# Performance work log

Measured on AMD Instinct MI355X. Metric: run time of the kernel, lower is better.

Reference implementation:

```python
import jax, jax.numpy as jnp
import numpy as np

B = 16384          # batch
N_IN = 1024        # input nodes
L = 8              # layers
W_LAYER = 512      # nodes per layer (fan-in and fan-out)
N_NODES = N_IN + L * W_LAYER  # 5120 total nodes in shared buffer
MASK_DENSITY = 0.25


def setup_inputs() -> dict:
    key = jax.random.key(0)
    kx, kw, km, kb = jax.random.split(key, 4)
    x = jax.random.normal(kx, (B, N_IN), dtype=jnp.float32)
    W = jax.random.normal(kw, (L, W_LAYER, W_LAYER), dtype=jnp.float32) * 0.05
    mask = (jax.random.uniform(km, (L, W_LAYER, W_LAYER)) < MASK_DENSITY).astype(jnp.float32)
    bias = jax.random.normal(kb, (L, W_LAYER), dtype=jnp.float32) * 0.01
    rng = np.random.default_rng(0)
    # layer l gathers from nodes already computed: indices in [0, N_IN + l*W_LAYER)
    in_idx = np.stack([rng.integers(0, N_IN + l * W_LAYER, size=W_LAYER) for l in range(L)]).astype(np.int32)
    # layer l writes its own contiguous node slots
    out_idx = np.stack([np.arange(N_IN + l * W_LAYER, N_IN + (l + 1) * W_LAYER) for l in range(L)]).astype(np.int32)
    return {"x": x, "W": W, "mask": mask, "bias": bias,
            "in_idx": jnp.asarray(in_idx), "out_idx": jnp.asarray(out_idx)}


def reference(x, W, mask, bias, in_idx, out_idx):
    # shared node-value buffer, inputs written into first N_IN columns
    values = jnp.zeros((x.shape[0], N_NODES), dtype=x.dtype)
    values = values.at[:, :N_IN].set(x)

    def step(vals, layer):
        idx_in, idx_out, Wl, ml, bl = layer
        node_inputs = vals[:, idx_in]                       # [B, W_LAYER] gather
        h = jax.nn.relu(node_inputs @ (Wl * ml).T + bl)     # masked linear + ReLU
        return vals.at[:, idx_out].set(h), None             # scatter back

    values, _ = jax.lax.scan(step, values, (in_idx, out_idx, W, mask, bias))
    return values[:, out_idx[-1]]  # output nodes = last layer's nodes
```

## Files before the change

### kernel.cpp

```cpp
#include <hip/hip_runtime.h>
#include <stdint.h>

typedef unsigned short u16;
typedef unsigned int   u32;
typedef short s16x8 __attribute__((ext_vector_type(8)));
typedef float f32x4 __attribute__((ext_vector_type(4)));

#define NB    16384
#define NIN   1024
#define WLY   512
#define NLAY  8
#define NNODE (NIN + NLAY * WLY)
#define BN    64

__device__ __forceinline__ u16 f2bf(float f) {
  union { float f; u32 u; } c; c.f = f;
  return (u16)((c.u + 0x7fffu + ((c.u >> 16) & 1u)) >> 16);
}
__device__ __forceinline__ float bf2f(u16 h) {
  union { u32 u; float f; } c; c.u = ((u32)h) << 16;
  return c.f;
}

#define SCHED0() __builtin_amdgcn_sched_barrier(0)
#define BAR()    __builtin_amdgcn_s_barrier()
#define WAITLG0() asm volatile("s_waitcnt lgkmcnt(0)" ::: "memory")

__global__ void prep_w(const float* __restrict__ W, const float* __restrict__ Mk,
                       u16* __restrict__ Wm) {
  int id   = blockIdx.x * 256 + threadIdx.x;
  int lane = id & 63;
  int chunk = id >> 6;
  int kf = chunk & 1;
  int mb = (chunk >> 1) & 31;
  int kt = (chunk >> 6) & 7;
  int l  = chunk >> 9;
  int m  = (mb << 4) + (lane & 15);
  int k0 = (kt << 6) + (kf << 5) + ((lane >> 4) << 3);
  size_t base = ((size_t)l << 18) + (size_t)m * 512 + k0;
  const float4* w4 = (const float4*)(W + base);
  const float4* k4 = (const float4*)(Mk + base);
  float4 w0 = w4[0], w1 = w4[1];
  float4 k0v = k4[0], k1v = k4[1];
  u32 p0 = (u32)f2bf(w0.x * k0v.x) | ((u32)f2bf(w0.y * k0v.y) << 16);
  u32 p1 = (u32)f2bf(w0.z * k0v.z) | ((u32)f2bf(w0.w * k0v.w) << 16);
  u32 p2 = (u32)f2bf(w1.x * k1v.x) | ((u32)f2bf(w1.y * k1v.y) << 16);
  u32 p3 = (u32)f2bf(w1.z * k1v.z) | ((u32)f2bf(w1.w * k1v.w) << 16);
  uint4 v; v.x = p0; v.y = p1; v.z = p2; v.w = p3;
  *(uint4*)(Wm + ((size_t)chunk << 9) + (lane << 3)) = v;
}

__global__ __launch_bounds__(512, 2) void fused_net(
    const float* __restrict__ x, const u16* __restrict__ Wfrag,
    const float* __restrict__ bias, const int* __restrict__ in_idx,
    u16* __restrict__ V, float* __restrict__ out) {

  __shared__ __align__(16) u16 Graw[2][64 * 72];
  __shared__ __align__(16) u16 Gswz[4][4096];
  __shared__ __align__(16) u16 Ebuf[512 * 72];

  int t = threadIdx.x;
  int lane = t & 63, w = t >> 6;
  int mlane = lane & 15, g = lane >> 4;
  int n0 = blockIdx.x * BN;
  int krow  = (w << 3) + (lane >> 3);
  int kcol8 = lane & 7;

  float* xt = (float*)Ebuf;
  for (int cc = 0; cc < 8; ++cc) {
    #pragma unroll
    for (int it = 0; it < 4; ++it) {
      int cl = t + it * 512;
      int b = cl >> 5, p = cl & 31;
      *(float4*)(xt + b * 128 + (p << 2)) =
          *(const float4*)(x + (size_t)(n0 + b) * 1024 + cc * 128 + (p << 2));
    }
    __syncthreads();
    {
      int c = t >> 2, seg = t & 3;
      u32 p[8];
      #pragma unroll
      for (int i = 0; i < 8; ++i) {
        u16 lo = f2bf(xt[(seg * 16 + 2 * i) * 128 + c]);
        u16 hi = f2bf(xt[(seg * 16 + 2 * i + 1) * 128 + c]);
        p[i] = (u32)lo | ((u32)hi << 16);
      }
      u16* dst = V + (size_t)(cc * 128 + c) * NB + n0 + seg * 16;
      uint4 v0; v0.x = p[0]; v0.y = p[1]; v0.z = p[2]; v0.w = p[3];
      uint4 v1; v1.x = p[4]; v1.y = p[5]; v1.z = p[6]; v1.w = p[7];
      *(uint4*)dst = v0;
      *(uint4*)(dst + 8) = v1;
    }
    __syncthreads();
  }

#define GLD(KT) do {                                                           \
    gv[(KT) & 3] =                                                             \
        *(const uint4*)(V + (size_t)rowv[KT] * NB + n0 + (kcol8 << 3));        \
  } while (0)

#define STW(KT) do {                                                           \
    *(uint4*)((char*)Graw[(KT) & 1] + krow * 144 + (kcol8 << 4)) =             \
        gv[(KT) & 3];                                                          \
  } while (0)

#define TRANSP(KT) do {                                                        \
    const u16* gb_ = Graw[(KT) & 1];                                           \
    u32 p0_ = (u32)gb_[(w * 8 + 0) * 72 + lane] |                              \
              ((u32)gb_[(w * 8 + 1) * 72 + lane] << 16);                       \
    u32 p1_ = (u32)gb_[(w * 8 + 2) * 72 + lane] |                              \
              ((u32)gb_[(w * 8 + 3) * 72 + lane] << 16);                       \
    u32 p2_ = (u32)gb_[(w * 8 + 4) * 72 + lane] |                              \
              ((u32)gb_[(w * 8 + 5) * 72 + lane] << 16);                       \
    u32 p3_ = (u32)gb_[(w * 8 + 6) * 72 + lane] |                              \
              ((u32)gb_[(w * 8 + 7) * 72 + lane] << 16);                       \
    uint4 vv_; vv_.x = p0_; vv_.y = p1_; vv_.z = p2_; vv_.w = p3_;             \
    *(uint4*)((char*)Gswz[(KT) & 3] + lane * 128 +                             \
              ((w * 16) ^ ((lane & 7) << 4))) = vv_;                           \
  } while (0)

#define LDA(KTN) do {                                                          \
    _Pragma("unroll") for (int mb = 0; mb < 4; ++mb)                           \
    _Pragma("unroll") for (int kf = 0; kf < 2; ++kf)                           \
      a[(KTN) & 3][mb][kf] = *(const s16x8*)(Wl +                              \
          ((size_t)((((KTN) * 32 + (w << 2) + mb) << 1) + kf) << 9) +          \
          (lane << 3));                                                        \
  } while (0)

#define MM(KT) do {                                                            \
    const char* gs_ = (const char*)Gswz[(KT) & 3];                             \
    _Pragma("unroll") for (int kf = 0; kf < 2; ++kf) {                         \
      s16x8 bfr[4];                                                            \
      _Pragma("unroll") for (int nf = 0; nf < 4; ++nf) {                       \
        int n_ = (nf << 4) + mlane;                                            \
        bfr[nf] = *(const s16x8*)(gs_ + n_ * 128 +                             \
                  (((kf << 6) + (g << 4)) ^ ((n_ & 7) << 4)));                 \
      }                                                                        \
      _Pragma("unroll") for (int mb = 0; mb < 4; ++mb)                         \
      _Pragma("unroll") for (int nf = 0; nf < 4; ++nf)                         \
        acc[mb][nf] = __builtin_amdgcn_mfma_f32_16x16x32_bf16(                 \
            a[(KT) & 3][mb][kf], bfr[nf], acc[mb][nf], 0, 0, 0);               \
    }                                                                          \
  } while (0)

  for (int l = 0; l < NLAY; ++l) {
    __syncthreads();

    int rowv[8];
    #pragma unroll
    for (int kt = 0; kt < 8; ++kt)
      rowv[kt] = in_idx[(l << 9) + (kt << 6) + krow];

    const u16* Wl = Wfrag + ((size_t)l << 18);
    int node_out = NIN + l * WLY;

    f32x4 acc[4][4];
    #pragma unroll
    for (int i = 0; i < 4; ++i)
      #pragma unroll
      for (int j = 0; j < 4; ++j)
        acc[i][j] = (f32x4){0.f, 0.f, 0.f, 0.f};

    s16x8 a[4][4][2];
    uint4 gv[4];

    GLD(0); GLD(1);
    LDA(0); LDA(1);
    STW(0); STW(1);
    TRANSP(0); TRANSP(1);
    GLD(2); GLD(3);
    SCHED0(); WAITLG0(); BAR(); SCHED0();

    GLD(4); GLD(5);
    LDA(2); LDA(3);
    MM(0); MM(1);
    STW(2); STW(3);
    TRANSP(2); TRANSP(3);
    SCHED0(); WAITLG0(); BAR(); SCHED0();

    GLD(6); GLD(7);
    LDA(4); LDA(5);
    MM(2); MM(3);
    STW(4); STW(5);
    TRANSP(4); TRANSP(5);
    SCHED0(); WAITLG0(); BAR(); SCHED0();

    LDA(6); LDA(7);
    MM(4); MM(5);
    STW(6); STW(7);
    TRANSP(6); TRANSP(7);
    SCHED0(); WAITLG0(); BAR(); SCHED0();

    MM(6); MM(7);

    if (l < NLAY - 1) {
      #pragma unroll
      for (int mb = 0; mb < 4; ++mb) {
        float4 bv = *(const float4*)(bias + (l << 9) + (w << 6) + (mb << 4) + (g << 2));
        float bvr[4] = {bv.x, bv.y, bv.z, bv.w};
        #pragma unroll
        for (int nf = 0; nf < 4; ++nf)
          #pragma unroll
          for (int r = 0; r < 4; ++r) {
            int m = (w << 6) + (mb << 4) + (g << 2) + r;
            int n = (nf << 4) + mlane;
            Ebuf[m * 72 + n] = f2bf(fmaxf(acc[mb][nf][r] + bvr[r], 0.f));
          }
      }
      #pragma unroll
      for (int it = 0; it < 8; ++it) {
        int row = (w << 6) + (it << 3) + (lane >> 3);
        uint4 vv = *(uint4*)(Ebuf + row * 72 + ((lane & 7) << 3));
        *(uint4*)(V + (size_t)(node_out + row) * NB + n0 + ((lane & 7) << 3)) = vv;
      }
    } else {
      #pragma unroll
      for (int mb = 0; mb < 4; ++mb) {
        float4 bv = *(const float4*)(bias + (l << 9) + (w << 6) + (mb << 4) + (g << 2));
        float bvr[4] = {bv.x, bv.y, bv.z, bv.w};
        #pragma unroll
        for (int nf = 0; nf < 4; ++nf)
          #pragma unroll
          for (int r = 0; r < 4; ++r) {
            int m = (w << 6) + (mb << 4) + (g << 2) + r;
            int n = (nf << 4) + mlane;
            Ebuf[m * 66 + n] = f2bf(fmaxf(acc[mb][nf][r] + bvr[r], 0.f));
          }
      }
      __syncthreads();
      #pragma unroll
      for (int pn = 0; pn < 8; ++pn)
        #pragma unroll
        for (int h = 0; h < 2; ++h) {
          int n = (t >> 6) + (pn << 3);
          int mbase = ((t & 63) << 2) + (h << 8);
          float4 v;
          v.x = bf2f(Ebuf[(mbase + 0) * 66 + n]);
          v.y = bf2f(Ebuf[(mbase + 1) * 66 + n]);
          v.z = bf2f(Ebuf[(mbase + 2) * 66 + n]);
          v.w = bf2f(Ebuf[(mbase + 3) * 66 + n]);
          *(float4*)(out + (size_t)(n0 + n) * 512 + mbase) = v;
        }
    }
  }
#undef GLD
#undef STW
#undef TRANSP
#undef LDA
#undef MM
}

extern "C" void kernel_launch(void* const* d_in, const int* in_sizes, int n_in,
                              void* d_out, int out_size, void* d_ws, size_t ws_size,
                              hipStream_t stream) {
  (void)in_sizes; (void)n_in; (void)out_size; (void)ws_size;
  const float* x    = (const float*)d_in[0];
  const float* W    = (const float*)d_in[1];
  const float* Mk   = (const float*)d_in[2];
  const float* bias = (const float*)d_in[3];
  const int*  inidx = (const int*)d_in[4];
  float* out = (float*)d_out;

  char* ws = (char*)d_ws;
  u16* V     = (u16*)ws;
  u16* Wfrag = (u16*)(ws + (size_t)NNODE * NB * 2);

  prep_w<<<dim3(1024), 256, 0, stream>>>(W, Mk, Wfrag);
  fused_net<<<dim3(256), 512, 0, stream>>>(x, Wfrag, bias, inidx, V, out);
}
```

Baseline: 108.8 us.

## Double fused_net block to 1024 threads, halve per-wave rows, prefetch next indices

The fused network kernel now runs with 16 waves per block instead of 8. Each wave owns 32 output rows instead of 64 and moves half-width slices of the gathered activations, so accumulator and A-fragment register arrays shrink to keep more waves resident. Weight-fragment loads are now interleaved one k-tile ahead with the MFMA steps rather than staged two at a time. Next-layer gather indices are prefetched during the current layer's matmul. The aim is more latency hiding per CU, at the cost of narrower 8-byte global and LDS accesses and a launch bound that may force tighter register limits or spills.

```diff
diff --git a/kernel.cpp b/kernel.cpp
--- a/kernel.cpp
+++ b/kernel.cpp
@@ -50,7 +50,7 @@
   *(uint4*)(Wm + ((size_t)chunk << 9) + (lane << 3)) = v;
 }
 
-__global__ __launch_bounds__(512, 2) void fused_net(
+__global__ __launch_bounds__(1024, 4) void fused_net(
     const float* __restrict__ x, const u16* __restrict__ Wfrag,
     const float* __restrict__ bias, const int* __restrict__ in_idx,
     u16* __restrict__ V, float* __restrict__ out) {
@@ -63,67 +63,60 @@
   int lane = t & 63, w = t >> 6;
   int mlane = lane & 15, g = lane >> 4;
   int n0 = blockIdx.x * BN;
-  int krow  = (w << 3) + (lane >> 3);
-  int kcol8 = lane & 7;
+  int krow  = (w << 2) + (lane >> 4);
+  int kcol4 = lane & 15;
 
   float* xt = (float*)Ebuf;
   for (int cc = 0; cc < 8; ++cc) {
     #pragma unroll
-    for (int it = 0; it < 4; ++it) {
-      int cl = t + it * 512;
+    for (int it = 0; it < 2; ++it) {
+      int cl = t + it * 1024;
       int b = cl >> 5, p = cl & 31;
       *(float4*)(xt + b * 128 + (p << 2)) =
           *(const float4*)(x + (size_t)(n0 + b) * 1024 + cc * 128 + (p << 2));
     }
     __syncthreads();
     {
-      int c = t >> 2, seg = t & 3;
-      u32 p[8];
-      #pragma unroll
-      for (int i = 0; i < 8; ++i) {
-        u16 lo = f2bf(xt[(seg * 16 + 2 * i) * 128 + c]);
-        u16 hi = f2bf(xt[(seg * 16 + 2 * i + 1) * 128 + c]);
+      int c = t >> 3, seg = t & 7;
+      u32 p[4];
+      #pragma unroll
+      for (int i = 0; i < 4; ++i) {
+        u16 lo = f2bf(xt[(seg * 8 + 2 * i) * 128 + c]);
+        u16 hi = f2bf(xt[(seg * 8 + 2 * i + 1) * 128 + c]);
         p[i] = (u32)lo | ((u32)hi << 16);
       }
-      u16* dst = V + (size_t)(cc * 128 + c) * NB + n0 + seg * 16;
-      uint4 v0; v0.x = p[0]; v0.y = p[1]; v0.z = p[2]; v0.w = p[3];
-      uint4 v1; v1.x = p[4]; v1.y = p[5]; v1.z = p[6]; v1.w = p[7];
-      *(uint4*)dst = v0;
-      *(uint4*)(dst + 8) = v1;
+      uint4 vv; vv.x = p[0]; vv.y = p[1]; vv.z = p[2]; vv.w = p[3];
+      *(uint4*)(V + (size_t)(cc * 128 + c) * NB + n0 + (seg << 3)) = vv;
     }
     __syncthreads();
   }
 
 #define GLD(KT) do {                                                           \
     gv[(KT) & 3] =                                                             \
-        *(const uint4*)(V + (size_t)rowv[KT] * NB + n0 + (kcol8 << 3));        \
+        *(const uint2*)(V + (size_t)rowv[KT] * NB + n0 + (kcol4 << 2));        \
   } while (0)
 
 #define STW(KT) do {                                                           \
-    *(uint4*)((char*)Graw[(KT) & 1] + krow * 144 + (kcol8 << 4)) =             \
+    *(uint2*)((char*)Graw[(KT) & 1] + krow * 144 + (kcol4 << 3)) =             \
         gv[(KT) & 3];                                                          \
   } while (0)
 
 #define TRANSP(KT) do {                                                        \
     const u16* gb_ = Graw[(KT) & 1];                                           \
-    u32 p0_ = (u32)gb_[(w * 8 + 0) * 72 + lane] |                              \
-              ((u32)gb_[(w * 8 + 1) * 72 + lane] << 16);                       \
-    u32 p1_ = (u32)gb_[(w * 8 + 2) * 72 + lane] |                              \
-              ((u32)gb_[(w * 8 + 3) * 72 + lane] << 16);                       \
-    u32 p2_ = (u32)gb_[(w * 8 + 4) * 72 + lane] |                              \
-              ((u32)gb_[(w * 8 + 5) * 72 + lane] << 16);                       \
-    u32 p3_ = (u32)gb_[(w * 8 + 6) * 72 + lane] |                              \
-              ((u32)gb_[(w * 8 + 7) * 72 + lane] << 16);                       \
-    uint4 vv_; vv_.x = p0_; vv_.y = p1_; vv_.z = p2_; vv_.w = p3_;             \
-    *(uint4*)((char*)Gswz[(KT) & 3] + lane * 128 +                             \
-              ((w * 16) ^ ((lane & 7) << 4))) = vv_;                           \
+    u32 p0_ = (u32)gb_[(w * 4 + 0) * 72 + lane] |                              \
+              ((u32)gb_[(w * 4 + 1) * 72 + lane] << 16);                       \
+    u32 p1_ = (u32)gb_[(w * 4 + 2) * 72 + lane] |                              \
+              ((u32)gb_[(w * 4 + 3) * 72 + lane] << 16);                       \
+    uint2 vv_; vv_.x = p0_; vv_.y = p1_;                                       \
+    *(uint2*)((char*)Gswz[(KT) & 3] + lane * 128 +                             \
+              ((w * 8) ^ ((lane & 7) << 4))) = vv_;                            \
   } while (0)
 
 #define LDA(KTN) do {                                                          \
-    _Pragma("unroll") for (int mb = 0; mb < 4; ++mb)                           \
+    _Pragma("unroll") for (int mb = 0; mb < 2; ++mb)                           \
     _Pragma("unroll") for (int kf = 0; kf < 2; ++kf)                           \
-      a[(KTN) & 3][mb][kf] = *(const s16x8*)(Wl +                              \
-          ((size_t)((((KTN) * 32 + (w << 2) + mb) << 1) + kf) << 9) +          \
+      a[mb][kf] = *(const s16x8*)(Wl +                                         \
+          ((size_t)((((KTN) * 32 + (w << 1) + mb) << 1) + kf) << 9) +          \
           (lane << 3));                                                        \
   } while (0)
 
@@ -136,10 +129,10 @@
         bfr[nf] = *(const s16x8*)(gs_ + n_ * 128 +                             \
                   (((kf << 6) + (g << 4)) ^ ((n_ & 7) << 4)));                 \
       }                                                                        \
-      _Pragma("unroll") for (int mb = 0; mb < 4; ++mb)                         \
+      _Pragma("unroll") for (int mb = 0; mb < 2; ++mb)                         \
       _Pragma("unroll") for (int nf = 0; nf < 4; ++nf)                         \
         acc[mb][nf] = __builtin_amdgcn_mfma_f32_16x16x32_bf16(                 \
-            a[(KT) & 3][mb][kf], bfr[nf], acc[mb][nf], 0, 0, 0);               \
+            a[mb][kf], bfr[nf], acc[mb][nf], 0, 0, 0);                         \
     }                                                                          \
   } while (0)
 
@@ -154,85 +147,98 @@
     const u16* Wl = Wfrag + ((size_t)l << 18);
     int node_out = NIN + l * WLY;
 
-    f32x4 acc[4][4];
-    #pragma unroll
-    for (int i = 0; i < 4; ++i)
+    f32x4 acc[2][4];
+    #pragma unroll
+    for (int i = 0; i < 2; ++i)
       #pragma unroll
       for (int j = 0; j < 4; ++j)
         acc[i][j] = (f32x4){0.f, 0.f, 0.f, 0.f};
 
-    s16x8 a[4][4][2];
-    uint4 gv[4];
-
-    GLD(0); GLD(1);
-    LDA(0); LDA(1);
+    s16x8 a[2][2];
+    uint2 gv[4];
+
+    GLD(0); GLD(1); GLD(2); GLD(3);
+    LDA(0);
     STW(0); STW(1);
     TRANSP(0); TRANSP(1);
-    GLD(2); GLD(3);
-    SCHED0(); WAITLG0(); BAR(); SCHED0();
+    SCHED0(); WAITLG0(); BAR(); SCHED0();
+
+    int rowvn[8];
+    if (l + 1 < NLAY) {
+      #pragma unroll
+      for (int kt = 0; kt < 8; ++kt)
+        rowvn[kt] = in_idx[((l + 1) << 9) + (kt << 6) + krow];
+    } else {
+      #pragma unroll
+      for (int kt = 0; kt < 8; ++kt) rowvn[kt] = 0;
+    }
 
     GLD(4); GLD(5);
-    LDA(2); LDA(3);
-    MM(0); MM(1);
+    MM(0); LDA(1);
+    MM(1); LDA(2);
     STW(2); STW(3);
     TRANSP(2); TRANSP(3);
     SCHED0(); WAITLG0(); BAR(); SCHED0();
 
     GLD(6); GLD(7);
-    LDA(4); LDA(5);
-    MM(2); MM(3);
+    MM(2); LDA(3);
+    MM(3); LDA(4);
     STW(4); STW(5);
     TRANSP(4); TRANSP(5);
     SCHED0(); WAITLG0(); BAR(); SCHED0();
 
-    LDA(6); LDA(7);
-    MM(4); MM(5);
+    MM(4); LDA(5);
+    MM(5); LDA(6);
     STW(6); STW(7);
     TRANSP(6); TRANSP(7);
     SCHED0(); WAITLG0(); BAR(); SCHED0();
 
-    MM(6); MM(7);
+    MM(6); LDA(7);
+    MM(7);
+
+    #pragma unroll
+    for (int kt = 0; kt < 8; ++kt) rowv[kt] = rowvn[kt];
 
     if (l < NLAY - 1) {
       #pragma unroll
-      for (int mb = 0; mb < 4; ++mb) {
-        float4 bv = *(const float4*)(bias + (l << 9) + (w << 6) + (mb << 4) + (g << 2));
+      for (int mb = 0; mb < 2; ++mb) {
+        float4 bv = *(const float4*)(bias + (l << 9) + (w << 5) + (mb << 4) + (g << 2));
         float bvr[4] = {bv.x, bv.y, bv.z, bv.w};
         #pragma unroll
         for (int nf = 0; nf < 4; ++nf)
           #pragma unroll
           for (int r = 0; r < 4; ++r) {
-            int m = (w << 6) + (mb << 4) + (g << 2) + r;
+            int m = (w << 5) + (mb << 4) + (g << 2) + r;
             int n = (nf << 4) + mlane;
             Ebuf[m * 72 + n] = f2bf(fmaxf(acc[mb][nf][r] + bvr[r], 0.f));
           }
       }
       #pragma unroll
-      for (int it = 0; it < 8; ++it) {
-        int row = (w << 6) + (it << 3) + (lane >> 3);
+      for (int it = 0; it < 4; ++it) {
+        int row = (w << 5) + (it << 3) + (lane >> 3);
         uint4 vv = *(uint4*)(Ebuf + row * 72 + ((lane & 7) << 3));
         *(uint4*)(V + (size_t)(node_out + row) * NB + n0 + ((lane & 7) << 3)) = vv;
       }
     } else {
       #pragma unroll
-      for (int mb = 0; mb < 4; ++mb) {
-        float4 bv = *(const float4*)(bias + (l << 9) + (w << 6) + (mb << 4) + (g << 2));
+      for (int mb = 0; mb < 2; ++mb) {
+        float4 bv = *(const float4*)(bias + (l << 9) + (w << 5) + (mb << 4) + (g << 2));
         float bvr[4] = {bv.x, bv.y, bv.z, bv.w};
         #pragma unroll
         for (int nf = 0; nf < 4; ++nf)
           #pragma unroll
           for (int r = 0; r < 4; ++r) {
-            int m = (w << 6) + (mb << 4) + (g << 2) + r;
+            int m = (w << 5) + (mb << 4) + (g << 2) + r;
             int n = (nf << 4) + mlane;
             Ebuf[m * 66 + n] = f2bf(fmaxf(acc[mb][nf][r] + bvr[r], 0.f));
           }
       }
       __syncthreads();
       #pragma unroll
-      for (int pn = 0; pn < 8; ++pn)
+      for (int pn = 0; pn < 4; ++pn)
         #pragma unroll
         for (int h = 0; h < 2; ++h) {
-          int n = (t >> 6) + (pn << 3);
+          int n = (t >> 6) + (pn << 4);
           int mbase = ((t & 63) << 2) + (h << 8);
           float4 v;
           v.x = bf2f(Ebuf[(mbase + 0) * 66 + n]);
@@ -266,5 +272,5 @@
   u16* Wfrag = (u16*)(ws + (size_t)NNODE * NB * 2);
 
   prep_w<<<dim3(1024), 256, 0, stream>>>(W, Mk, Wfrag);
-  fused_net<<<dim3(256), 512, 0, stream>>>(x, Wfrag, bias, inidx, V, out);
-}
+  fused_net<<<dim3(256), 1024, 0, stream>>>(x, Wfrag, bias, inidx, V, out);
+}
```

Result: no change. 109.7 us (+0.8%).

## Halve batch tile to 32 columns with 4-wave blocks and more grid blocks

Applied to the files above, without the earlier changes.

Shrinks each block's batch tile from 64 to 32 columns and from 8 waves to 4, launching 512 blocks instead of 256 so the 256 CUs receive more work. Block indices are remapped so that paired blocks cover adjacent 32-column halves. Each wave now owns 8 M-fragments with 2 N-fragments, and the weight fragments are loaded just before each MFMA step instead of being double-buffered ahead. The next layer's gather indices are prefetched during the current layer. In exchange, each block reads the full weight matrix for only half as many batch columns, which doubles total weight traffic, and the weight load latency is less hidden.

```diff
diff --git a/kernel.cpp b/kernel.cpp
--- a/kernel.cpp
+++ b/kernel.cpp
@@ -11,7 +11,7 @@
 #define WLY   512
 #define NLAY  8
 #define NNODE (NIN + NLAY * WLY)
-#define BN    64
+#define BN    32
 
 __device__ __forceinline__ u16 f2bf(float f) {
   union { float f; u32 u; } c; c.f = f;
@@ -50,34 +50,34 @@
   *(uint4*)(Wm + ((size_t)chunk << 9) + (lane << 3)) = v;
 }
 
-__global__ __launch_bounds__(512, 2) void fused_net(
+__global__ __launch_bounds__(256, 2) void fused_net(
     const float* __restrict__ x, const u16* __restrict__ Wfrag,
     const float* __restrict__ bias, const int* __restrict__ in_idx,
     u16* __restrict__ V, float* __restrict__ out) {
 
-  __shared__ __align__(16) u16 Graw[2][64 * 72];
-  __shared__ __align__(16) u16 Gswz[4][4096];
-  __shared__ __align__(16) u16 Ebuf[512 * 72];
+  __shared__ __align__(16) u16 Graw[2][64 * 40];
+  __shared__ __align__(16) u16 Gswz[4][2048];
+  __shared__ __align__(16) u16 Ebuf[512 * 40];
 
   int t = threadIdx.x;
   int lane = t & 63, w = t >> 6;
   int mlane = lane & 15, g = lane >> 4;
-  int n0 = blockIdx.x * BN;
-  int krow  = (w << 3) + (lane >> 3);
-  int kcol8 = lane & 7;
+  int n0 = ((blockIdx.x & 255) << 6) + ((blockIdx.x >> 8) << 5);
+  int krow = (w << 4) + (lane >> 2);
+  int kcol = lane & 3;
 
   float* xt = (float*)Ebuf;
   for (int cc = 0; cc < 8; ++cc) {
     #pragma unroll
     for (int it = 0; it < 4; ++it) {
-      int cl = t + it * 512;
+      int cl = t + it * 256;
       int b = cl >> 5, p = cl & 31;
       *(float4*)(xt + b * 128 + (p << 2)) =
           *(const float4*)(x + (size_t)(n0 + b) * 1024 + cc * 128 + (p << 2));
     }
     __syncthreads();
     {
-      int c = t >> 2, seg = t & 3;
+      int c = t >> 1, seg = t & 1;
       u32 p[8];
       #pragma unroll
       for (int i = 0; i < 8; ++i) {
@@ -96,50 +96,51 @@
 
 #define GLD(KT) do {                                                           \
     gv[(KT) & 3] =                                                             \
-        *(const uint4*)(V + (size_t)rowv[KT] * NB + n0 + (kcol8 << 3));        \
+        *(const uint4*)(V + (size_t)rowv[KT] * NB + n0 + (kcol << 3));         \
   } while (0)
 
 #define STW(KT) do {                                                           \
-    *(uint4*)((char*)Graw[(KT) & 1] + krow * 144 + (kcol8 << 4)) =             \
-        gv[(KT) & 3];                                                          \
+    *(uint4*)((char*)Graw[(KT) & 1] + krow * 80 + (kcol << 4)) = gv[(KT) & 3]; \
   } while (0)
 
 #define TRANSP(KT) do {                                                        \
     const u16* gb_ = Graw[(KT) & 1];                                           \
-    u32 p0_ = (u32)gb_[(w * 8 + 0) * 72 + lane] |                              \
-              ((u32)gb_[(w * 8 + 1) * 72 + lane] << 16);                       \
-    u32 p1_ = (u32)gb_[(w * 8 + 2) * 72 + lane] |                              \
-              ((u32)gb_[(w * 8 + 3) * 72 + lane] << 16);                       \
-    u32 p2_ = (u32)gb_[(w * 8 + 4) * 72 + lane] |                              \
-              ((u32)gb_[(w * 8 + 5) * 72 + lane] << 16);                       \
-    u32 p3_ = (u32)gb_[(w * 8 + 6) * 72 + lane] |                              \
-              ((u32)gb_[(w * 8 + 7) * 72 + lane] << 16);                       \
+    int n_ = lane & 31, rg_ = lane >> 5;                                       \
+    int rb_ = (w << 4) + (rg_ << 3);                                           \
+    u32 p0_ = (u32)gb_[(rb_ + 0) * 40 + n_] |                                  \
+              ((u32)gb_[(rb_ + 1) * 40 + n_] << 16);                           \
+    u32 p1_ = (u32)gb_[(rb_ + 2) * 40 + n_] |                                  \
+              ((u32)gb_[(rb_ + 3) * 40 + n_] << 16);                           \
+    u32 p2_ = (u32)gb_[(rb_ + 4) * 40 + n_] |                                  \
+              ((u32)gb_[(rb_ + 5) * 40 + n_] << 16);                           \
+    u32 p3_ = (u32)gb_[(rb_ + 6) * 40 + n_] |                                  \
+              ((u32)gb_[(rb_ + 7) * 40 + n_] << 16);                           \
     uint4 vv_; vv_.x = p0_; vv_.y = p1_; vv_.z = p2_; vv_.w = p3_;             \
-    *(uint4*)((char*)Gswz[(KT) & 3] + lane * 128 +                             \
-              ((w * 16) ^ ((lane & 7) << 4))) = vv_;                           \
+    *(uint4*)((char*)Gswz[(KT) & 3] + n_ * 128 +                               \
+              (((w << 5) + (rg_ << 4)) ^ ((n_ & 7) << 4))) = vv_;              \
   } while (0)
 
 #define LDA(KTN) do {                                                          \
-    _Pragma("unroll") for (int mb = 0; mb < 4; ++mb)                           \
+    _Pragma("unroll") for (int mb = 0; mb < 8; ++mb)                           \
     _Pragma("unroll") for (int kf = 0; kf < 2; ++kf)                           \
-      a[(KTN) & 3][mb][kf] = *(const s16x8*)(Wl +                              \
-          ((size_t)((((KTN) * 32 + (w << 2) + mb) << 1) + kf) << 9) +          \
+      a[mb][kf] = *(const s16x8*)(Wl +                                         \
+          ((size_t)((((KTN) * 32 + (w << 3) + mb) << 1) + kf) << 9) +          \
           (lane << 3));                                                        \
   } while (0)
 
 #define MM(KT) do {                                                            \
     const char* gs_ = (const char*)Gswz[(KT) & 3];                             \
     _Pragma("unroll") for (int kf = 0; kf < 2; ++kf) {                         \
-      s16x8 bfr[4];                                                            \
-      _Pragma("unroll") for (int nf = 0; nf < 4; ++nf) {                       \
+      s16x8 bfr[2];                                                            \
+      _Pragma("unroll") for (int nf = 0; nf < 2; ++nf) {                       \
         int n_ = (nf << 4) + mlane;                                            \
         bfr[nf] = *(const s16x8*)(gs_ + n_ * 128 +                             \
                   (((kf << 6) + (g << 4)) ^ ((n_ & 7) << 4)));                 \
       }                                                                        \
-      _Pragma("unroll") for (int mb = 0; mb < 4; ++mb)                         \
-      _Pragma("unroll") for (int nf = 0; nf < 4; ++nf)                         \
+      _Pragma("unroll") for (int mb = 0; mb < 8; ++mb)                         \
+      _Pragma("unroll") for (int nf = 0; nf < 2; ++nf)                         \
         acc[mb][nf] = __builtin_amdgcn_mfma_f32_16x16x32_bf16(                 \
-            a[(KT) & 3][mb][kf], bfr[nf], acc[mb][nf], 0, 0, 0);               \
+            a[mb][kf], bfr[nf], acc[mb][nf], 0, 0, 0);                         \
     }                                                                          \
   } while (0)
 
@@ -154,77 +155,90 @@
     const u16* Wl = Wfrag + ((size_t)l << 18);
     int node_out = NIN + l * WLY;
 
-    f32x4 acc[4][4];
-    #pragma unroll
-    for (int i = 0; i < 4; ++i)
-      #pragma unroll
-      for (int j = 0; j < 4; ++j)
+    f32x4 acc[8][2];
+    #pragma unroll
+    for (int i = 0; i < 8; ++i)
+      #pragma unroll
+      for (int j = 0; j < 2; ++j)
         acc[i][j] = (f32x4){0.f, 0.f, 0.f, 0.f};
 
-    s16x8 a[4][4][2];
+    s16x8 a[8][2];
     uint4 gv[4];
 
     GLD(0); GLD(1);
-    LDA(0); LDA(1);
     STW(0); STW(1);
     TRANSP(0); TRANSP(1);
     GLD(2); GLD(3);
     SCHED0(); WAITLG0(); BAR(); SCHED0();
 
+    int rowvn[8];
+    if (l + 1 < NLAY) {
+      #pragma unroll
+      for (int kt = 0; kt < 8; ++kt)
+        rowvn[kt] = in_idx[((l + 1) << 9) + (kt << 6) + krow];
+    } else {
+      #pragma unroll
+      for (int kt = 0; kt < 8; ++kt) rowvn[kt] = 0;
+    }
+
     GLD(4); GLD(5);
-    LDA(2); LDA(3);
-    MM(0); MM(1);
+    LDA(0); MM(0);
+    LDA(1); MM(1);
     STW(2); STW(3);
     TRANSP(2); TRANSP(3);
     SCHED0(); WAITLG0(); BAR(); SCHED0();
 
     GLD(6); GLD(7);
-    LDA(4); LDA(5);
-    MM(2); MM(3);
+    LDA(2); MM(2);
+    LDA(3); MM(3);
     STW(4); STW(5);
     TRANSP(4); TRANSP(5);
     SCHED0(); WAITLG0(); BAR(); SCHED0();
 
-    LDA(6); LDA(7);
-    MM(4); MM(5);
+    LDA(4); MM(4);
+    LDA(5); MM(5);
     STW(6); STW(7);
     TRANSP(6); TRANSP(7);
     SCHED0(); WAITLG0(); BAR(); SCHED0();
 
-    MM(6); MM(7);
+    LDA(6); MM(6);
+    LDA(7); MM(7);
+
+    #pragma unroll
+    for (int kt = 0; kt < 8; ++kt) rowv[kt] = rowvn[kt];
 
     if (l < NLAY - 1) {
       #pragma unroll
-      for (int mb = 0; mb < 4; ++mb) {
-        float4 bv = *(const float4*)(bias + (l << 9) + (w << 6) + (mb << 4) + (g << 2));
+      for (int mb = 0; mb < 8; ++mb) {
+        float4 bv = *(const float4*)(bias + (l << 9) + (w << 7) + (mb << 4) + (g << 2));
         float bvr[4] = {bv.x, bv.y, bv.z, bv.w};
         #pragma unroll
-        for (int nf = 0; nf < 4; ++nf)
+        for (int nf = 0; nf < 2; ++nf)
           #pragma unroll
           for (int r = 0; r < 4; ++r) {
-            int m = (w << 6) + (mb << 4) + (g << 2) + r;
+            int m = (w << 7) + (mb << 4) + (g << 2) + r;
             int n = (nf << 4) + mlane;
-            Ebuf[m * 72 + n] = f2bf(fmaxf(acc[mb][nf][r] + bvr[r], 0.f));
+            Ebuf[m * 40 + n] = f2bf(fmaxf(acc[mb][nf][r] + bvr[r], 0.f));
           }
       }
       #pragma unroll
       for (int it = 0; it < 8; ++it) {
-        int row = (w << 6) + (it << 3) + (lane >> 3);
-        uint4 vv = *(uint4*)(Ebuf + row * 72 + ((lane & 7) << 3));
-        *(uint4*)(V + (size_t)(node_out + row) * NB + n0 + ((lane & 7) << 3)) = vv;
+        int row = (w << 7) + (it << 4) + (lane >> 2);
+        uint4 vv = *(uint4*)(Ebuf + row * 40 + (kcol << 3));
+        *(uint4*)(V + (size_t)(node_out + row) * NB + n0 + (kcol << 3)) = vv;
       }
     } else {
       #pragma unroll
-      for (int mb = 0; mb < 4; ++mb) {
-        float4 bv = *(const float4*)(bias + (l << 9) + (w << 6) + (mb << 4) + (g << 2));
+      for (int mb = 0; mb < 8; ++mb) {
+        float4 bv = *(const float4*)(bias + (l << 9) + (w << 7) + (mb << 4) + (g << 2));
         float bvr[4] = {bv.x, bv.y, bv.z, bv.w};
         #pragma unroll
-        for (int nf = 0; nf < 4; ++nf)
+        for (int nf = 0; nf < 2; ++nf)
           #pragma unroll
           for (int r = 0; r < 4; ++r) {
-            int m = (w << 6) + (mb << 4) + (g << 2) + r;
+            int m = (w << 7) + (mb << 4) + (g << 2) + r;
             int n = (nf << 4) + mlane;
-            Ebuf[m * 66 + n] = f2bf(fmaxf(acc[mb][nf][r] + bvr[r], 0.f));
+            Ebuf[m * 40 + n] = f2bf(fmaxf(acc[mb][nf][r] + bvr[r], 0.f));
           }
       }
       __syncthreads();
@@ -232,13 +246,13 @@
       for (int pn = 0; pn < 8; ++pn)
         #pragma unroll
         for (int h = 0; h < 2; ++h) {
-          int n = (t >> 6) + (pn << 3);
+          int n = (t >> 6) + (pn << 2);
           int mbase = ((t & 63) << 2) + (h << 8);
           float4 v;
-          v.x = bf2f(Ebuf[(mbase + 0) * 66 + n]);
-          v.y = bf2f(Ebuf[(mbase + 1) * 66 + n]);
-          v.z = bf2f(Ebuf[(mbase + 2) * 66 + n]);
-          v.w = bf2f(Ebuf[(mbase + 3) * 66 + n]);
+          v.x = bf2f(Ebuf[(mbase + 0) * 40 + n]);
+          v.y = bf2f(Ebuf[(mbase + 1) * 40 + n]);
+          v.z = bf2f(Ebuf[(mbase + 2) * 40 + n]);
+          v.w = bf2f(Ebuf[(mbase + 3) * 40 + n]);
           *(float4*)(out + (size_t)(n0 + n) * 512 + mbase) = v;
         }
     }
@@ -266,5 +280,5 @@
   u16* Wfrag = (u16*)(ws + (size_t)NNODE * NB * 2);
 
   prep_w<<<dim3(1024), 256, 0, stream>>>(W, Mk, Wfrag);
-  fused_net<<<dim3(256), 512, 0, stream>>>(x, Wfrag, bias, inidx, V, out);
-}
+  fused_net<<<dim3(512), 256, 0, stream>>>(x, Wfrag, bias, inidx, V, out);
+}
```

Result: slower. 232.2 us (+113.4%).
